# Optimization experiments

Hardware: AMD Instinct MI355X
Metric: run time of the kernel (lower is better)

## Reference

```python
import jax, jax.numpy as jnp
import numpy as np

B, S, D = 2, 2048, 1024
H, Dh = 16, 64  # qkv_features=1024, head_dim=64
F = 1024        # out_features


def setup_inputs() -> dict:
    key = jax.random.key(0)
    ks = jax.random.split(key, 16)
    s = 0.02
    return {
        'inputs_q': jax.random.normal(ks[0], (B, S, D), jnp.float32),
        'inputs_kv': jax.random.normal(ks[1], (B, S, D), jnp.float32),
        'pos_embed': jax.random.normal(ks[2], (S, D), jnp.float32),
        'Wq': jax.random.normal(ks[3], (D, H, Dh), jnp.float32) * s,
        'bq': jnp.zeros((H, Dh), jnp.float32),
        'Wk': jax.random.normal(ks[4], (D, H, Dh), jnp.float32) * s,
        'bk': jnp.zeros((H, Dh), jnp.float32),
        'Wv': jax.random.normal(ks[5], (D, H, Dh), jnp.float32) * s,
        'bv': jnp.zeros((H, Dh), jnp.float32),
        'Wpos': jax.random.normal(ks[6], (D, H, Dh), jnp.float32) * s,
        'r_r_bias': jax.random.normal(ks[7], (H, Dh), jnp.float32) * s,
        'r_w_bias': jax.random.normal(ks[8], (H, Dh), jnp.float32) * s,
        'Wout': jax.random.normal(ks[9], (H, Dh, F), jnp.float32) * s,
        'bout': jnp.zeros((F,), jnp.float32),
    }


_roll_vmap = jax.vmap(jnp.roll, in_axes=(-2, 0, None), out_axes=-2)


def reference(inputs_q, inputs_kv, pos_embed, Wq, bq, Wk, bk, Wv, bv,
              Wpos, r_r_bias, r_w_bias, Wout, bout):
    # QKV projections: [B,S,D] x [D,H,Dh] -> [B,S,H,Dh]
    q = jnp.einsum('bsd,dhk->bshk', inputs_q, Wq) + bq
    k = jnp.einsum('bsd,dhk->bshk', inputs_kv, Wk) + bk
    v = jnp.einsum('bsd,dhk->bshk', inputs_kv, Wv) + bv
    # relative position embedding projection: [S,D] -> [S,H,Dh]
    r_pos = jnp.einsum('sd,dhk->shk', pos_embed, Wpos)

    q_len = q.shape[-3]
    depth = q.shape[-1]
    # content score + relative-position score, both [B,H,S,S]
    aw = jnp.einsum('bqhd,bkhd->bhqk', q + r_w_bias, k)
    aw_r = jnp.einsum('bqhd,khd->bhqk', q + r_r_bias, r_pos)
    # Transformer-XL relative shift: per query-row roll along key axis
    shifts = jnp.arange(0, q_len) - (q_len - 1)
    aw_r = _roll_vmap(aw_r, shifts, -1)
    aw = (aw + aw_r) / jnp.sqrt(depth).astype(aw.dtype)
    attn = jax.nn.softmax(aw, axis=-1)
    # weighted sum: [B,S,H,Dh]
    x = jnp.einsum('bhqk,bkhd->bqhd', attn, v)
    # output projection contracting (H,Dh)
    out = jnp.einsum('bqhd,hdf->bqf', x, Wout) + bout
    return out
```

## Files before the change

kernel.cpp:

```cpp
#include <hip/hip_runtime.h>
#include <hip/hip_bf16.h>
#include <hip/hip_fp16.h>


#define B_  2
#define S_  2048
#define D_  1024
#define H_  16
#define DH_ 64
#define HD_ 1024
#define F_  1024
#define N_  4096
#define SP_ 2056

typedef __attribute__((ext_vector_type(8))) short  short8;
typedef __attribute__((ext_vector_type(4))) float  floatx4;

__device__ __forceinline__ unsigned short f2bf(float x) {
  unsigned u = __float_as_uint(x);
  u += 0x7FFFu + ((u >> 16) & 1u);
  return (unsigned short)(u >> 16);
}
__device__ __forceinline__ unsigned short f2h(float x) {
  __half h = __float2half(x);
  unsigned short u; __builtin_memcpy(&u, &h, 2);
  return u;
}
__device__ __forceinline__ float h2f(unsigned short u) {
  __half h; __builtin_memcpy(&h, &u, 2);
  return __half2float(h);
}

#define CQ_ (N_ * D_ / 4)
__global__ void cast_all(const float* __restrict__ sq, const float* __restrict__ skv,
                         const float* __restrict__ spos,
                         unsigned short* __restrict__ dq, unsigned short* __restrict__ dkv,
                         unsigned short* __restrict__ dpos) {
  int i = blockIdx.x * blockDim.x + threadIdx.x;
  const float* s; unsigned short* d; int off;
  if (i < CQ_)            { s = sq;   d = dq;   off = i; }
  else if (i < 2 * CQ_)   { s = skv;  d = dkv;  off = i - CQ_; }
  else                    { s = spos; d = dpos; off = i - 2 * CQ_; }
  float4 v = ((const float4*)s)[off];
  ushort4 o = make_ushort4(f2bf(v.x), f2bf(v.y), f2bf(v.z), f2bf(v.w));
  ((ushort4*)d)[off] = o;
}

struct TP5 { const float* s[5]; unsigned short* d[5]; };
__global__ void transpose_all(TP5 p) {
  __shared__ float t[32][33];
  const float* src = p.s[blockIdx.z];
  unsigned short* dst = p.d[blockIdx.z];
  int c0 = blockIdx.x * 32, r0 = blockIdx.y * 32;
  int tx = threadIdx.x, ty = threadIdx.y;
#pragma unroll
  for (int i = 0; i < 4; i++)
    t[ty + i * 8][tx] = src[(size_t)(r0 + ty + i * 8) * 1024 + c0 + tx];
  __syncthreads();
#pragma unroll
  for (int i = 0; i < 4; i++)
    dst[(size_t)(c0 + ty + i * 8) * 1024 + r0 + tx] = f2bf(t[tx][ty + i * 8]);
}

__launch_bounds__(256, 2)
__global__ void gemm_bt(const unsigned short* A, const unsigned short* Bt,
                        const float* bias, const float* b2a, const float* b2b,
                        unsigned short* outA, unsigned short* outB, float* outF,
                        int Nn, int K, int mode, int split,
                        const unsigned short* A2, const unsigned short* Bt2,
                        const float* bias2, unsigned short* outA2, int mode2) {
  __shared__ unsigned short As[128 * 64];
  __shared__ unsigned short Bs[128 * 64];
  int bx = blockIdx.x;
  if (split && bx >= split) {
    bx -= split; A = A2; Bt = Bt2; bias = bias2; outA = outA2; mode = mode2;
    b2a = nullptr; b2b = nullptr;
  }
  int nb = Nn >> 7;
  int bm = bx / nb, bn = bx % nb;
  int tid = threadIdx.x;
  int lane = tid & 63, wv = tid >> 6;
  int wm = wv >> 1, wn = wv & 1;
  int lm = lane & 15, lg = lane >> 4;
  const unsigned short* Ab = A + (size_t)(bm * 128) * K;
  const unsigned short* Bb = Bt + (size_t)(bn * 128) * K;
  floatx4 acc[4][4];
#pragma unroll
  for (int i = 0; i < 4; i++)
#pragma unroll
    for (int j = 0; j < 4; j++) acc[i][j] = (floatx4){0.f, 0.f, 0.f, 0.f};

  int lr = tid >> 3;
  int lc = (tid & 7) * 8;
  for (int k0 = 0; k0 < K; k0 += 64) {
    __syncthreads();
#pragma unroll
    for (int i = 0; i < 4; i++) {
      int r = i * 32 + lr;
      *(uint4*)&As[r * 64 + lc] = *(const uint4*)&Ab[(size_t)r * K + k0 + lc];
      *(uint4*)&Bs[r * 64 + lc] = *(const uint4*)&Bb[(size_t)r * K + k0 + lc];
    }
    __syncthreads();
#pragma unroll
    for (int kk = 0; kk < 2; kk++) {
      short8 af[4], bf[4];
#pragma unroll
      for (int i = 0; i < 4; i++)
        af[i] = *(const short8*)&As[(wm * 64 + i * 16 + lm) * 64 + kk * 32 + lg * 8];
#pragma unroll
      for (int j = 0; j < 4; j++)
        bf[j] = *(const short8*)&Bs[(wn * 64 + j * 16 + lm) * 64 + kk * 32 + lg * 8];
#pragma unroll
      for (int i = 0; i < 4; i++)
#pragma unroll
        for (int j = 0; j < 4; j++)
          acc[i][j] = __builtin_amdgcn_mfma_f32_16x16x32_bf16(af[i], bf[j], acc[i][j], 0, 0, 0);
    }
  }
#pragma unroll
  for (int j = 0; j < 4; j++) {
    int col = bn * 128 + wn * 64 + j * 16 + lm;
    float bs = bias ? bias[col] : 0.f;
    float ba = b2a ? b2a[col] : 0.f;
    float bb = b2b ? b2b[col] : 0.f;
#pragma unroll
    for (int i = 0; i < 4; i++) {
      int row0 = bm * 128 + wm * 64 + i * 16 + lg * 4;
      if (mode == 4) {
        int s = row0 & 2047, bb2 = row0 >> 11;
        size_t vidx = (((size_t)bb2 * H_ + (col >> 6)) * 64 + (col & 63)) * (size_t)S_ + s;
        ushort4 o = make_ushort4(f2bf(acc[i][j][0] + bs), f2bf(acc[i][j][1] + bs),
                                 f2bf(acc[i][j][2] + bs), f2bf(acc[i][j][3] + bs));
        *(ushort4*)&outA[vidx] = o;
      } else {
#pragma unroll
        for (int r = 0; r < 4; r++) {
          float v = acc[i][j][r] + bs;
          size_t idx = (size_t)(row0 + r) * Nn + col;
          if (mode == 0)      outA[idx] = f2bf(v);
          else if (mode == 1) { outA[idx] = f2bf(v + ba); outB[idx] = f2bf(v + bb); }
          else                outF[idx] = v;
        }
      }
    }
  }
}

__launch_bounds__(1024, 4)
__global__ void attn_kernel(const unsigned short* __restrict__ qw,
                            const unsigned short* __restrict__ qr,
                            const unsigned short* __restrict__ kb,
                            const unsigned short* __restrict__ rb,
                            const unsigned short* __restrict__ vt,
                            unsigned short* __restrict__ xb) {
  __shared__ __align__(16) unsigned short sS[32 * SP_];
  __shared__ float sLinv[32];
  int bid = blockIdx.x;
  int qt = bid & 63;
  int bh = bid >> 6;
  int b = bh >> 4, h = bh & 15;
  int q0 = qt * 32;
  int tid = threadIdx.x;
  int lane = tid & 63, wv = tid >> 6;
  int lm = lane & 15, lg = lane >> 4;

  short8 bqw[2][2], bqr[2][2];
  const size_t qbase = (size_t)(b * S_ + q0) * HD_ + h * 64;
#pragma unroll
  for (int t = 0; t < 2; t++) {
    const unsigned short* p1 = qw + qbase + (size_t)(t * 16 + lm) * HD_ + lg * 8;
    const unsigned short* p2 = qr + qbase + (size_t)(t * 16 + lm) * HD_ + lg * 8;
    bqw[t][0] = *(const short8*)(p1);
    bqw[t][1] = *(const short8*)(p1 + 32);
    bqr[t][0] = *(const short8*)(p2);
    bqr[t][1] = *(const short8*)(p2 + 32);
  }

#pragma unroll 2
  for (int jt = 0; jt < 8; jt++) {
    int jb = wv * 128 + jt * 16;
    const unsigned short* rp = rb + (size_t)(jb + lm) * HD_ + h * 64 + lg * 8;
    short8 a0 = *(const short8*)(rp);
    short8 a1 = *(const short8*)(rp + 32);
#pragma unroll
    for (int t = 0; t < 2; t++) {
      floatx4 c = (floatx4){0.f, 0.f, 0.f, 0.f};
      c = __builtin_amdgcn_mfma_f32_16x16x32_bf16(a0, bqr[t][0], c, 0, 0, 0);
      c = __builtin_amdgcn_mfma_f32_16x16x32_bf16(a1, bqr[t][1], c, 0, 0, 0);
      int q = t * 16 + lm;
      int kbase = jb + lg * 4 + q0 + q + 1;
      unsigned short* row = &sS[q * SP_];
#pragma unroll
      for (int r = 0; r < 4; r++) row[(kbase + r) & 2047] = f2h(c[r]);
    }
  }
  __syncthreads();
#pragma unroll 2
  for (int kt = 0; kt < 8; kt++) {
    int kbb = wv * 128 + kt * 16;
    const unsigned short* kp = kb + (size_t)(b * S_ + kbb + lm) * HD_ + h * 64 + lg * 8;
    short8 a0 = *(const short8*)(kp);
    short8 a1 = *(const short8*)(kp + 32);
#pragma unroll
    for (int t = 0; t < 2; t++) {
      floatx4 c = (floatx4){0.f, 0.f, 0.f, 0.f};
      c = __builtin_amdgcn_mfma_f32_16x16x32_bf16(a0, bqw[t][0], c, 0, 0, 0);
      c = __builtin_amdgcn_mfma_f32_16x16x32_bf16(a1, bqw[t][1], c, 0, 0, 0);
      int q = t * 16 + lm;
      int kk = kbb + lg * 4;
      ushort4* p = (ushort4*)&sS[q * SP_ + kk];
      ushort4 u = *p;
      __half2 lo, hi;
      __builtin_memcpy(&lo, &u, 4);
      __builtin_memcpy(&hi, (char*)&u + 4, 4);
      lo = __hadd2(lo, __floats2half2_rn(c[0], c[1]));
      hi = __hadd2(hi, __floats2half2_rn(c[2], c[3]));
      ushort4 o;
      __builtin_memcpy(&o, &lo, 4);
      __builtin_memcpy((char*)&o + 4, &hi, 4);
      *p = o;
    }
  }
  __syncthreads();
  {
    int q = tid >> 5, ix = tid & 31;
    unsigned short* row = &sS[q * SP_];
    float sum = 0.f;
#pragma unroll 4
    for (int i = 0; i < 8; i++) {
      int k = (ix + 32 * i) * 8;
      short8 u = *(short8*)&row[k];
      short8 o;
#pragma unroll
      for (int e = 0; e < 8; e++) {
        float p = exp2f(h2f((unsigned short)u[e]) * 0.1803368801111204f);
        sum += p;
        o[e] = (short)f2bf(p);
      }
      *(short8*)&row[k] = o;
    }
#pragma unroll
    for (int d = 1; d < 32; d <<= 1) sum += __shfl_xor(sum, d);
    if (ix == 0) sLinv[q] = 1.f / sum;
  }
  __syncthreads();
  floatx4 acc[2][4];
#pragma unroll
  for (int m = 0; m < 2; m++)
#pragma unroll
    for (int j = 0; j < 4; j++) acc[m][j] = (floatx4){0.f, 0.f, 0.f, 0.f};
  const unsigned short* vb0 = vt + (size_t)(b * H_ + h) * 64 * S_;
#pragma unroll
  for (int s = 0; s < 4; s++) {
    int k0 = wv * 128 + s * 32;
    short8 a0 = *(short8*)&sS[lm * SP_ + k0 + lg * 8];
    short8 a1 = *(short8*)&sS[(16 + lm) * SP_ + k0 + lg * 8];
#pragma unroll
    for (int j = 0; j < 4; j++) {
      short8 bb = *(const short8*)&vb0[(size_t)(j * 16 + lm) * S_ + k0 + lg * 8];
      acc[0][j] = __builtin_amdgcn_mfma_f32_16x16x32_bf16(a0, bb, acc[0][j], 0, 0, 0);
      acc[1][j] = __builtin_amdgcn_mfma_f32_16x16x32_bf16(a1, bb, acc[1][j], 0, 0, 0);
    }
  }
  __syncthreads();
  float* po = (float*)sS;
#pragma unroll
  for (int m = 0; m < 2; m++)
#pragma unroll
    for (int j = 0; j < 4; j++)
#pragma unroll
      for (int r = 0; r < 4; r++) {
        int q = m * 16 + lg * 4 + r;
        int dh = j * 16 + lm;
        po[wv * 2048 + q * 64 + dh] = acc[m][j][r];
      }
  __syncthreads();
  {
    int e = tid * 2;
    int q = e >> 6, dh = e & 63;
    float2 v = *(float2*)&po[e];
#pragma unroll
    for (int w = 1; w < 16; w++) {
      float2 u = *(float2*)&po[w * 2048 + e];
      v.x += u.x; v.y += u.y;
    }
    float li = sLinv[q];
    ushort2 o = make_ushort2(f2bf(v.x * li), f2bf(v.y * li));
    *(ushort2*)&xb[(size_t)(b * S_ + q0 + q) * HD_ + h * 64 + dh] = o;
  }
}

extern "C" void kernel_launch(void* const* d_in, const int* in_sizes, int n_in,
                              void* d_out, int out_size, void* d_ws, size_t ws_size,
                              hipStream_t stream) {
  const float* inputs_q  = (const float*)d_in[0];
  const float* inputs_kv = (const float*)d_in[1];
  const float* pos_embed = (const float*)d_in[2];
  const float* Wq   = (const float*)d_in[3];
  const float* bq   = (const float*)d_in[4];
  const float* Wk   = (const float*)d_in[5];
  const float* bk   = (const float*)d_in[6];
  const float* Wv   = (const float*)d_in[7];
  const float* bv   = (const float*)d_in[8];
  const float* Wpos = (const float*)d_in[9];
  const float* rrb  = (const float*)d_in[10];
  const float* rwb  = (const float*)d_in[11];
  const float* Wout = (const float*)d_in[12];
  const float* bout = (const float*)d_in[13];
  float* out = (float*)d_out;

  char* ws = (char*)d_ws;
  unsigned short* aq  = (unsigned short*)(ws);
  unsigned short* akv = (unsigned short*)(ws + ( 8u << 20));
  unsigned short* apo = (unsigned short*)(ws + (16u << 20));
  unsigned short* wqt = (unsigned short*)(ws + (20u << 20));
  unsigned short* wkt = (unsigned short*)(ws + (22u << 20));
  unsigned short* wvt = (unsigned short*)(ws + (24u << 20));
  unsigned short* wpt = (unsigned short*)(ws + (26u << 20));
  unsigned short* wot = (unsigned short*)(ws + (28u << 20));
  unsigned short* qwp = (unsigned short*)(ws + (30u << 20));
  unsigned short* qrp = (unsigned short*)(ws + (38u << 20));
  unsigned short* kbp = (unsigned short*)(ws + (46u << 20));
  unsigned short* vtp = (unsigned short*)(ws + (54u << 20));
  unsigned short* rbp = (unsigned short*)(ws + (62u << 20));
  unsigned short* xbp = aq;

  cast_all<<<10240, 256, 0, stream>>>(inputs_q, inputs_kv, pos_embed, aq, akv, apo);
  TP5 tp;
  tp.s[0] = Wq; tp.s[1] = Wk; tp.s[2] = Wv; tp.s[3] = Wpos; tp.s[4] = Wout;
  tp.d[0] = wqt; tp.d[1] = wkt; tp.d[2] = wvt; tp.d[3] = wpt; tp.d[4] = wot;
  transpose_all<<<dim3(32, 32, 5), dim3(32, 8), 0, stream>>>(tp);

  gemm_bt<<<256 + 128, 256, 0, stream>>>(aq, wqt, bq, rwb, rrb, qwp, qrp, nullptr,
                                         HD_, D_, 1, 256, apo, wpt, nullptr, rbp, 0);
  gemm_bt<<<512, 256, 0, stream>>>(akv, wkt, bk, nullptr, nullptr, kbp, nullptr, nullptr,
                                   HD_, D_, 0, 256, akv, wvt, bv, vtp, 4);
  attn_kernel<<<2048, 1024, 0, stream>>>(qwp, qrp, kbp, rbp, vtp, xbp);
  gemm_bt<<<256, 256, 0, stream>>>(xbp, wot, bout, nullptr, nullptr, nullptr, nullptr, out,
                                   F_, HD_, 2, 0, nullptr, nullptr, nullptr, nullptr, 0);
}
```

Baseline: 498.2 us.

## Chunk attention keys into double-buffered LDS tiles and fuse softmax exp

Restructures the attention kernel to process keys in four 512-wide chunks with two smaller LDS score buffers instead of one full 2048-wide row buffer. The exp is fused into the content-score pass, and P·V accumulates per chunk. The block size halves to 512 threads, and the smaller LDS footprint is meant to allow more resident blocks per CU. In exchange, some relative-position tiles are recomputed at chunk boundaries and there are more barriers.

```diff
diff --git a/kernel.cpp b/kernel.cpp
--- a/kernel.cpp
+++ b/kernel.cpp
@@ -11,7 +11,8 @@
 #define HD_ 1024
 #define F_  1024
 #define N_  4096
-#define SP_ 2056
+#define KC_ 512
+#define SP2 520
 
 typedef __attribute__((ext_vector_type(8))) short  short8;
 typedef __attribute__((ext_vector_type(4))) float  floatx4;
@@ -146,14 +147,15 @@
   }
 }
 
-__launch_bounds__(1024, 4)
+__launch_bounds__(512, 4)
 __global__ void attn_kernel(const unsigned short* __restrict__ qw,
                             const unsigned short* __restrict__ qr,
                             const unsigned short* __restrict__ kb,
                             const unsigned short* __restrict__ rb,
                             const unsigned short* __restrict__ vt,
                             unsigned short* __restrict__ xb) {
-  __shared__ __align__(16) unsigned short sS[32 * SP_];
+  __shared__ __align__(16) unsigned short sS[2][32 * SP2];
+  __shared__ float sSum[8][32];
   __shared__ float sLinv[32];
   int bid = blockIdx.x;
   int qt = bid & 63;
@@ -176,93 +178,88 @@
     bqr[t][1] = *(const short8*)(p2 + 32);
   }
 
+  floatx4 acc[2][4];
+#pragma unroll
+  for (int m = 0; m < 2; m++)
+#pragma unroll
+    for (int j = 0; j < 4; j++) acc[m][j] = (floatx4){0.f, 0.f, 0.f, 0.f};
+  float s0 = 0.f, s1 = 0.f;
+
+  const unsigned short* vb0 = vt + (size_t)(b * H_ + h) * 64 * S_;
+  const float KSC = 0.1803368801111204f;
+
+  for (int c = 0; c < 4; c++) {
+    unsigned short* S = sS[c & 1];
+    int kc = c * KC_;
+    for (int jt = wv; jt < 34; jt += 8) {
+      int jrow = (kc - q0 - 32 + jt * 16 + lm) & 2047;
+      const unsigned short* rp = rb + (size_t)jrow * HD_ + h * 64 + lg * 8;
+      short8 a0 = *(const short8*)(rp);
+      short8 a1 = *(const short8*)(rp + 32);
+#pragma unroll
+      for (int t = 0; t < 2; t++) {
+        floatx4 c4 = (floatx4){0.f, 0.f, 0.f, 0.f};
+        c4 = __builtin_amdgcn_mfma_f32_16x16x32_bf16(a0, bqr[t][0], c4, 0, 0, 0);
+        c4 = __builtin_amdgcn_mfma_f32_16x16x32_bf16(a1, bqr[t][1], c4, 0, 0, 0);
+        int q = t * 16 + lm;
+        int ub = jt * 16 + lg * 4 + q - 31;
+        unsigned short* row = &S[q * SP2];
+#pragma unroll
+        for (int r = 0; r < 4; r++) {
+          int u = ub + r;
+          if ((unsigned)u < (unsigned)KC_) row[u] = f2h(c4[r]);
+        }
+      }
+    }
+    __syncthreads();
 #pragma unroll 2
-  for (int jt = 0; jt < 8; jt++) {
-    int jb = wv * 128 + jt * 16;
-    const unsigned short* rp = rb + (size_t)(jb + lm) * HD_ + h * 64 + lg * 8;
-    short8 a0 = *(const short8*)(rp);
-    short8 a1 = *(const short8*)(rp + 32);
-#pragma unroll
-    for (int t = 0; t < 2; t++) {
-      floatx4 c = (floatx4){0.f, 0.f, 0.f, 0.f};
-      c = __builtin_amdgcn_mfma_f32_16x16x32_bf16(a0, bqr[t][0], c, 0, 0, 0);
-      c = __builtin_amdgcn_mfma_f32_16x16x32_bf16(a1, bqr[t][1], c, 0, 0, 0);
-      int q = t * 16 + lm;
-      int kbase = jb + lg * 4 + q0 + q + 1;
-      unsigned short* row = &sS[q * SP_];
-#pragma unroll
-      for (int r = 0; r < 4; r++) row[(kbase + r) & 2047] = f2h(c[r]);
-    }
-  }
+    for (int kt = 0; kt < 4; kt++) {
+      int u0 = wv * 64 + kt * 16;
+      const unsigned short* kp = kb + (size_t)(b * S_ + kc + u0 + lm) * HD_ + h * 64 + lg * 8;
+      short8 a0 = *(const short8*)(kp);
+      short8 a1 = *(const short8*)(kp + 32);
+#pragma unroll
+      for (int t = 0; t < 2; t++) {
+        floatx4 c4 = (floatx4){0.f, 0.f, 0.f, 0.f};
+        c4 = __builtin_amdgcn_mfma_f32_16x16x32_bf16(a0, bqw[t][0], c4, 0, 0, 0);
+        c4 = __builtin_amdgcn_mfma_f32_16x16x32_bf16(a1, bqw[t][1], c4, 0, 0, 0);
+        int q = t * 16 + lm;
+        ushort4* p = (ushort4*)&S[q * SP2 + u0 + lg * 4];
+        ushort4 Rv = *p;
+        float p0 = exp2f((c4[0] + h2f(Rv.x)) * KSC);
+        float p1 = exp2f((c4[1] + h2f(Rv.y)) * KSC);
+        float p2 = exp2f((c4[2] + h2f(Rv.z)) * KSC);
+        float p3 = exp2f((c4[3] + h2f(Rv.w)) * KSC);
+        float ps = (p0 + p1) + (p2 + p3);
+        if (t == 0) s0 += ps; else s1 += ps;
+        *p = make_ushort4(f2bf(p0), f2bf(p1), f2bf(p2), f2bf(p3));
+      }
+    }
+    __syncthreads();
+#pragma unroll
+    for (int s = 0; s < 2; s++) {
+      int u0 = wv * 64 + s * 32;
+      short8 a0 = *(short8*)&S[lm * SP2 + u0 + lg * 8];
+      short8 a1 = *(short8*)&S[(16 + lm) * SP2 + u0 + lg * 8];
+      const unsigned short* vp = vb0 + kc + u0 + lg * 8;
+#pragma unroll
+      for (int j = 0; j < 4; j++) {
+        short8 bb = *(const short8*)&vp[(size_t)(j * 16 + lm) * S_];
+        acc[0][j] = __builtin_amdgcn_mfma_f32_16x16x32_bf16(a0, bb, acc[0][j], 0, 0, 0);
+        acc[1][j] = __builtin_amdgcn_mfma_f32_16x16x32_bf16(a1, bb, acc[1][j], 0, 0, 0);
+      }
+    }
+  }
+  s0 += __shfl_xor(s0, 16); s0 += __shfl_xor(s0, 32);
+  s1 += __shfl_xor(s1, 16); s1 += __shfl_xor(s1, 32);
+  if (lane < 16) { sSum[wv][lane] = s0; sSum[wv][16 + lane] = s1; }
   __syncthreads();
-#pragma unroll 2
-  for (int kt = 0; kt < 8; kt++) {
-    int kbb = wv * 128 + kt * 16;
-    const unsigned short* kp = kb + (size_t)(b * S_ + kbb + lm) * HD_ + h * 64 + lg * 8;
-    short8 a0 = *(const short8*)(kp);
-    short8 a1 = *(const short8*)(kp + 32);
-#pragma unroll
-    for (int t = 0; t < 2; t++) {
-      floatx4 c = (floatx4){0.f, 0.f, 0.f, 0.f};
-      c = __builtin_amdgcn_mfma_f32_16x16x32_bf16(a0, bqw[t][0], c, 0, 0, 0);
-      c = __builtin_amdgcn_mfma_f32_16x16x32_bf16(a1, bqw[t][1], c, 0, 0, 0);
-      int q = t * 16 + lm;
-      int kk = kbb + lg * 4;
-      ushort4* p = (ushort4*)&sS[q * SP_ + kk];
-      ushort4 u = *p;
-      __half2 lo, hi;
-      __builtin_memcpy(&lo, &u, 4);
-      __builtin_memcpy(&hi, (char*)&u + 4, 4);
-      lo = __hadd2(lo, __floats2half2_rn(c[0], c[1]));
-      hi = __hadd2(hi, __floats2half2_rn(c[2], c[3]));
-      ushort4 o;
-      __builtin_memcpy(&o, &lo, 4);
-      __builtin_memcpy((char*)&o + 4, &hi, 4);
-      *p = o;
-    }
-  }
-  __syncthreads();
-  {
-    int q = tid >> 5, ix = tid & 31;
-    unsigned short* row = &sS[q * SP_];
-    float sum = 0.f;
-#pragma unroll 4
-    for (int i = 0; i < 8; i++) {
-      int k = (ix + 32 * i) * 8;
-      short8 u = *(short8*)&row[k];
-      short8 o;
-#pragma unroll
-      for (int e = 0; e < 8; e++) {
-        float p = exp2f(h2f((unsigned short)u[e]) * 0.1803368801111204f);
-        sum += p;
-        o[e] = (short)f2bf(p);
-      }
-      *(short8*)&row[k] = o;
-    }
-#pragma unroll
-    for (int d = 1; d < 32; d <<= 1) sum += __shfl_xor(sum, d);
-    if (ix == 0) sLinv[q] = 1.f / sum;
-  }
-  __syncthreads();
-  floatx4 acc[2][4];
-#pragma unroll
-  for (int m = 0; m < 2; m++)
-#pragma unroll
-    for (int j = 0; j < 4; j++) acc[m][j] = (floatx4){0.f, 0.f, 0.f, 0.f};
-  const unsigned short* vb0 = vt + (size_t)(b * H_ + h) * 64 * S_;
-#pragma unroll
-  for (int s = 0; s < 4; s++) {
-    int k0 = wv * 128 + s * 32;
-    short8 a0 = *(short8*)&sS[lm * SP_ + k0 + lg * 8];
-    short8 a1 = *(short8*)&sS[(16 + lm) * SP_ + k0 + lg * 8];
-#pragma unroll
-    for (int j = 0; j < 4; j++) {
-      short8 bb = *(const short8*)&vb0[(size_t)(j * 16 + lm) * S_ + k0 + lg * 8];
-      acc[0][j] = __builtin_amdgcn_mfma_f32_16x16x32_bf16(a0, bb, acc[0][j], 0, 0, 0);
-      acc[1][j] = __builtin_amdgcn_mfma_f32_16x16x32_bf16(a1, bb, acc[1][j], 0, 0, 0);
-    }
-  }
-  __syncthreads();
+  if (tid < 32) {
+    float t = 0.f;
+#pragma unroll
+    for (int w = 0; w < 8; w++) t += sSum[w][tid];
+    sLinv[tid] = 1.f / t;
+  }
   float* po = (float*)sS;
 #pragma unroll
   for (int m = 0; m < 2; m++)
@@ -276,17 +273,17 @@
       }
   __syncthreads();
   {
-    int e = tid * 2;
+    int e = tid * 4;
     int q = e >> 6, dh = e & 63;
-    float2 v = *(float2*)&po[e];
-#pragma unroll
-    for (int w = 1; w < 16; w++) {
-      float2 u = *(float2*)&po[w * 2048 + e];
-      v.x += u.x; v.y += u.y;
+    float4 v = *(float4*)&po[e];
+#pragma unroll
+    for (int w = 1; w < 8; w++) {
+      float4 u = *(float4*)&po[w * 2048 + e];
+      v.x += u.x; v.y += u.y; v.z += u.z; v.w += u.w;
     }
     float li = sLinv[q];
-    ushort2 o = make_ushort2(f2bf(v.x * li), f2bf(v.y * li));
-    *(ushort2*)&xb[(size_t)(b * S_ + q0 + q) * HD_ + h * 64 + dh] = o;
+    ushort4 o = make_ushort4(f2bf(v.x * li), f2bf(v.y * li), f2bf(v.z * li), f2bf(v.w * li));
+    *(ushort4*)&xb[(size_t)(b * S_ + q0 + q) * HD_ + h * 64 + dh] = o;
   }
 }
 
@@ -335,7 +332,7 @@
                                          HD_, D_, 1, 256, apo, wpt, nullptr, rbp, 0);
   gemm_bt<<<512, 256, 0, stream>>>(akv, wkt, bk, nullptr, nullptr, kbp, nullptr, nullptr,
                                    HD_, D_, 0, 256, akv, wvt, bv, vtp, 4);
-  attn_kernel<<<2048, 1024, 0, stream>>>(qwp, qrp, kbp, rbp, vtp, xbp);
+  attn_kernel<<<2048, 512, 0, stream>>>(qwp, qrp, kbp, rbp, vtp, xbp);
   gemm_bt<<<256, 256, 0, stream>>>(xbp, wot, bout, nullptr, nullptr, nullptr, nullptr, out,
                                    F_, HD_, 2, 0, nullptr, nullptr, nullptr, nullptr, 0);
 }
```

Result: faster. 433.0 us (-13.1%).
